# Kernel tuning notes

Hardware: AMD Instinct MI355X
Metric: run time of the kernel (lower is better)

Reference implementation:

```python
import jax, jax.numpy as jnp
import numpy as np

B, D, INNER, OUT = 8192, 256, 64, 256


def setup_inputs() -> dict:
    key = jax.random.key(0)
    ks = jax.random.split(key, 10)
    s = 0.1
    return {
        "x": jax.random.normal(ks[0], (B, D), dtype=jnp.float32),
        # per-feature inner MLPs: Linear(1, inner) -> ReLU -> Linear(inner, 1)
        "w1": jax.random.normal(ks[1], (D, INNER), dtype=jnp.float32) * s,
        "b1": jax.random.normal(ks[2], (D, INNER), dtype=jnp.float32) * s,
        "w2": jax.random.normal(ks[3], (D, INNER), dtype=jnp.float32) * s,
        "b2": jax.random.normal(ks[4], (D,), dtype=jnp.float32) * s,
        # outer MLP: Linear(D, inner) -> ReLU -> Linear(inner, out)
        "wo1": jax.random.normal(ks[5], (INNER, D), dtype=jnp.float32) * s,
        "bo1": jax.random.normal(ks[6], (INNER,), dtype=jnp.float32) * s,
        "wo2": jax.random.normal(ks[7], (OUT, INNER), dtype=jnp.float32) * s,
        "bo2": jax.random.normal(ks[8], (OUT,), dtype=jnp.float32) * s,
    }


def reference(x, w1, b1, w2, b2, wo1, bo1, wo2, bo2):
    # Vectorized per-feature tiny MLPs: h[b,d,i] = relu(x[b,d]*w1[d,i] + b1[d,i])
    h = jax.nn.relu(x[:, :, None] * w1[None, :, :] + b1[None, :, :])  # [B, D, INNER]
    inner = jnp.einsum('bdi,di->bd', h, w2) + b2[None, :]             # [B, D]
    # Outer MLP
    g = jax.nn.relu(inner @ wo1.T + bo1)                              # [B, INNER]
    return g @ wo2.T + bo2                                            # [B, OUT]
```

## Files before the change

kernel.cpp:

```cpp
#include <hip/hip_runtime.h>


#define B_TOT 8192
#define D_DIM 256
#define I_DIM 64
#define O_DIM 256
#define TB 8


__global__ __launch_bounds__(256)
void kal_prep(const float* __restrict__ w1, const float* __restrict__ b1,
              const float* __restrict__ w2, const float* __restrict__ wo1,
              const float* __restrict__ wo2, float4* __restrict__ ws) {
    int idx = blockIdx.x * 256 + threadIdx.x;
    if (idx < 16384) {
        int i = idx >> 8;
        int d = idx & 255;
        ws[idx] = make_float4(w1[d * I_DIM + i], b1[d * I_DIM + i],
                              w2[d * I_DIM + i], 0.0f);
    } else if (idx < 16384 + 4096) {
        int r  = idx - 16384;
        int dd = r >> 6;
        int j  = r & 63;
        ws[idx] = ((const float4*)wo1)[j * (D_DIM / 4) + dd];
    } else if (idx < 16384 + 8192) {
        int r  = idx - (16384 + 4096);
        int jj = r >> 8;
        int o  = r & 255;
        ws[idx] = ((const float4*)wo2)[o * (I_DIM / 4) + jj];
    }
}

__global__ __launch_bounds__(256)
void kal_main(const float* __restrict__ x,  const float* __restrict__ b2,
              const float* __restrict__ bo1, const float* __restrict__ bo2,
              const float4* __restrict__ ws, float* __restrict__ out) {
    const float4* pa = ws;
    const float4* pb = ws + 16384;
    const float4* pc = ws + 16384 + 4096;

    __shared__ float inner_s[TB][D_DIM];
    __shared__ float g_s[TB][I_DIM];

    const int t    = threadIdx.x;
    const int row0 = blockIdx.x * TB;

    {
        const int d = t;
        float xv[TB];
        #pragma unroll
        for (int b = 0; b < TB; ++b)
            xv[b] = x[(row0 + b) * D_DIM + d];

        float acc[TB];
        const float b2v = b2[d];
        #pragma unroll
        for (int b = 0; b < TB; ++b) acc[b] = b2v;

        #pragma unroll 8
        for (int i = 0; i < I_DIM; ++i) {
            const float4 w = pa[i * D_DIM + d];
            #pragma unroll
            for (int b = 0; b < TB; ++b) {
                float h = fmaf(xv[b], w.x, w.y);
                h = fmaxf(h, 0.0f);
                acc[b] = fmaf(h, w.z, acc[b]);
            }
        }
        #pragma unroll
        for (int b = 0; b < TB; ++b) inner_s[b][d] = acc[b];
    }
    __syncthreads();

    {
        const int j   = t & 63;
        const int grp = t >> 6;
        const float bo1v = bo1[j];
        float gacc[TB / 4];
        #pragma unroll
        for (int r = 0; r < TB / 4; ++r) gacc[r] = bo1v;

        #pragma unroll 4
        for (int dd = 0; dd < D_DIM / 4; ++dd) {
            const float4 wv = pb[dd * I_DIM + j];
            #pragma unroll
            for (int r = 0; r < TB / 4; ++r) {
                const int b = grp * (TB / 4) + r;
                float4 iv = ((const float4*)&inner_s[b][0])[dd];
                gacc[r] = fmaf(iv.x, wv.x, gacc[r]);
                gacc[r] = fmaf(iv.y, wv.y, gacc[r]);
                gacc[r] = fmaf(iv.z, wv.z, gacc[r]);
                gacc[r] = fmaf(iv.w, wv.w, gacc[r]);
            }
        }
        #pragma unroll
        for (int r = 0; r < TB / 4; ++r)
            g_s[grp * (TB / 4) + r][j] = fmaxf(gacc[r], 0.0f);
    }
    __syncthreads();

    {
        const int o = t;
        float oacc[TB];
        const float bo2v = bo2[o];
        #pragma unroll
        for (int b = 0; b < TB; ++b) oacc[b] = bo2v;

        #pragma unroll 4
        for (int jj = 0; jj < I_DIM / 4; ++jj) {
            const float4 wv = pc[jj * O_DIM + o];
            #pragma unroll
            for (int b = 0; b < TB; ++b) {
                float4 gv = ((const float4*)&g_s[b][0])[jj];
                oacc[b] = fmaf(gv.x, wv.x, oacc[b]);
                oacc[b] = fmaf(gv.y, wv.y, oacc[b]);
                oacc[b] = fmaf(gv.z, wv.z, oacc[b]);
                oacc[b] = fmaf(gv.w, wv.w, oacc[b]);
            }
        }
        #pragma unroll
        for (int b = 0; b < TB; ++b)
            out[(row0 + b) * O_DIM + o] = oacc[b];
    }
}

extern "C" void kernel_launch(void* const* d_in, const int* in_sizes, int n_in,
                              void* d_out, int out_size, void* d_ws, size_t ws_size,
                              hipStream_t stream) {
    const float* x   = (const float*)d_in[0];
    const float* w1  = (const float*)d_in[1];
    const float* b1  = (const float*)d_in[2];
    const float* w2  = (const float*)d_in[3];
    const float* b2  = (const float*)d_in[4];
    const float* wo1 = (const float*)d_in[5];
    const float* bo1 = (const float*)d_in[6];
    const float* wo2 = (const float*)d_in[7];
    const float* bo2 = (const float*)d_in[8];
    float* out = (float*)d_out;
    float4* ws = (float4*)d_ws;

    kal_prep<<<(24576 + 255) / 256, 256, 0, stream>>>(w1, b1, w2, wo1, wo2, ws);
    kal_main<<<B_TOT / TB, 256, 0, stream>>>(x, b2, bo1, bo2, ws, out);
}
```

Measured before the change: 101.6 us.

## Run outer MLP layers on bf16 MFMA with 16-row blocks

Replaces the scalar FMA loops for the two outer linear layers with bf16 16x16x32 MFMA instructions, pre-converting and re-laying out wo1/wo2 into bf16 fragment order in the prep kernel. Blocks now handle 16 rows with 512 threads, and the inner activations and hidden layer are stored in shared memory as bf16. This removes much of the VALU work outside the per-feature MLP, at the cost of reduced precision in the outer layers.

```diff
diff --git a/kernel.cpp b/kernel.cpp
--- a/kernel.cpp
+++ b/kernel.cpp
@@ -1,11 +1,17 @@
 #include <hip/hip_runtime.h>
+#include <hip/hip_bf16.h>
 
 
 #define B_TOT 8192
 #define D_DIM 256
 #define I_DIM 64
 #define O_DIM 256
-#define TB 8
+#define RB 16
+#define NT 512
+
+typedef __hip_bfloat16 bf16;
+using short8 = __attribute__((ext_vector_type(8))) short;
+using f32x4  = __attribute__((ext_vector_type(4))) float;
 
 
 __global__ __launch_bounds__(256)
@@ -18,109 +24,102 @@
         int d = idx & 255;
         ws[idx] = make_float4(w1[d * I_DIM + i], b1[d * I_DIM + i],
                               w2[d * I_DIM + i], 0.0f);
-    } else if (idx < 16384 + 4096) {
+    } else if (idx < 32768) {
         int r  = idx - 16384;
-        int dd = r >> 6;
-        int j  = r & 63;
-        ws[idx] = ((const float4*)wo1)[j * (D_DIM / 4) + dd];
-    } else if (idx < 16384 + 8192) {
-        int r  = idx - (16384 + 4096);
-        int jj = r >> 8;
-        int o  = r & 255;
-        ws[idx] = ((const float4*)wo2)[o * (I_DIM / 4) + jj];
+        int kc = r >> 11;
+        int rem = r & 2047;
+        int j  = rem >> 5;
+        int kk = rem & 31;
+        bf16* pbB = (bf16*)(ws + 16384);
+        pbB[r] = __float2bfloat16(wo1[j * D_DIM + kc * 32 + kk]);
+    } else if (idx < 49152) {
+        int r  = idx - 32768;
+        int kc = r >> 13;
+        int rem = r & 8191;
+        int o  = rem >> 5;
+        int kk = rem & 31;
+        bf16* pcB = (bf16*)(ws + 16384) + 16384;
+        pcB[r] = __float2bfloat16(wo2[o * I_DIM + kc * 32 + kk]);
     }
 }
 
-__global__ __launch_bounds__(256)
+__global__ __launch_bounds__(NT)
 void kal_main(const float* __restrict__ x,  const float* __restrict__ b2,
               const float* __restrict__ bo1, const float* __restrict__ bo2,
               const float4* __restrict__ ws, float* __restrict__ out) {
-    const float4* pa = ws;
-    const float4* pb = ws + 16384;
-    const float4* pc = ws + 16384 + 4096;
+    const float4* pa  = ws;
+    const bf16*   pbB = (const bf16*)(ws + 16384);
+    const bf16*   pcB = pbB + 16384;
 
-    __shared__ float inner_s[TB][D_DIM];
-    __shared__ float g_s[TB][I_DIM];
+    __shared__ bf16 inner_bf[RB][264];
+    __shared__ bf16 g_bf[RB][72];
 
     const int t    = threadIdx.x;
-    const int row0 = blockIdx.x * TB;
+    const int row0 = blockIdx.x * RB;
 
     {
-        const int d = t;
-        float xv[TB];
-        #pragma unroll
-        for (int b = 0; b < TB; ++b)
-            xv[b] = x[(row0 + b) * D_DIM + d];
-
-        float acc[TB];
+        const int d    = t & 255;
+        const int half = t >> 8;
+        float xv[8], acc[8];
         const float b2v = b2[d];
         #pragma unroll
-        for (int b = 0; b < TB; ++b) acc[b] = b2v;
-
-        #pragma unroll 8
+        for (int b = 0; b < 8; ++b) {
+            xv[b]  = x[(row0 + half * 8 + b) * D_DIM + d];
+            acc[b] = b2v;
+        }
+        #pragma unroll 4
         for (int i = 0; i < I_DIM; ++i) {
             const float4 w = pa[i * D_DIM + d];
             #pragma unroll
-            for (int b = 0; b < TB; ++b) {
+            for (int b = 0; b < 8; ++b) {
                 float h = fmaf(xv[b], w.x, w.y);
                 h = fmaxf(h, 0.0f);
                 acc[b] = fmaf(h, w.z, acc[b]);
             }
         }
         #pragma unroll
-        for (int b = 0; b < TB; ++b) inner_s[b][d] = acc[b];
+        for (int b = 0; b < 8; ++b)
+            inner_bf[half * 8 + b][d] = __float2bfloat16(acc[b]);
     }
     __syncthreads();
 
-    {
-        const int j   = t & 63;
-        const int grp = t >> 6;
-        const float bo1v = bo1[j];
-        float gacc[TB / 4];
+    const int lane = t & 63;
+    const int wave = t >> 6;
+    const int col  = lane & 15;
+    const int quad = lane >> 4;
+
+    if (wave < 4) {
+        const int j0 = wave * 16;
+        f32x4 acc = {0.f, 0.f, 0.f, 0.f};
         #pragma unroll
-        for (int r = 0; r < TB / 4; ++r) gacc[r] = bo1v;
-
-        #pragma unroll 4
-        for (int dd = 0; dd < D_DIM / 4; ++dd) {
-            const float4 wv = pb[dd * I_DIM + j];
-            #pragma unroll
-            for (int r = 0; r < TB / 4; ++r) {
-                const int b = grp * (TB / 4) + r;
-                float4 iv = ((const float4*)&inner_s[b][0])[dd];
-                gacc[r] = fmaf(iv.x, wv.x, gacc[r]);
-                gacc[r] = fmaf(iv.y, wv.y, gacc[r]);
-                gacc[r] = fmaf(iv.z, wv.z, gacc[r]);
-                gacc[r] = fmaf(iv.w, wv.w, gacc[r]);
-            }
+        for (int kc = 0; kc < 8; ++kc) {
+            short8 af = *(const short8*)&inner_bf[col][kc * 32 + quad * 8];
+            short8 bfr = *(const short8*)&pbB[(kc * 64 + j0 + col) * 32 + quad * 8];
+            acc = __builtin_amdgcn_mfma_f32_16x16x32_bf16(af, bfr, acc, 0, 0, 0);
         }
+        const float bo1v = bo1[j0 + col];
         #pragma unroll
-        for (int r = 0; r < TB / 4; ++r)
-            g_s[grp * (TB / 4) + r][j] = fmaxf(gacc[r], 0.0f);
+        for (int r = 0; r < 4; ++r) {
+            const int row = quad * 4 + r;
+            g_bf[row][j0 + col] = __float2bfloat16(fmaxf(acc[r] + bo1v, 0.0f));
+        }
     }
     __syncthreads();
 
-    {
-        const int o = t;
-        float oacc[TB];
-        const float bo2v = bo2[o];
+    #pragma unroll
+    for (int tile = 0; tile < 2; ++tile) {
+        const int o0 = wave * 16 + tile * 128;
+        f32x4 acc = {0.f, 0.f, 0.f, 0.f};
         #pragma unroll
-        for (int b = 0; b < TB; ++b) oacc[b] = bo2v;
-
-        #pragma unroll 4
-        for (int jj = 0; jj < I_DIM / 4; ++jj) {
-            const float4 wv = pc[jj * O_DIM + o];
-            #pragma unroll
-            for (int b = 0; b < TB; ++b) {
-                float4 gv = ((const float4*)&g_s[b][0])[jj];
-                oacc[b] = fmaf(gv.x, wv.x, oacc[b]);
-                oacc[b] = fmaf(gv.y, wv.y, oacc[b]);
-                oacc[b] = fmaf(gv.z, wv.z, oacc[b]);
-                oacc[b] = fmaf(gv.w, wv.w, oacc[b]);
-            }
+        for (int kc = 0; kc < 2; ++kc) {
+            short8 af = *(const short8*)&g_bf[col][kc * 32 + quad * 8];
+            short8 bfr = *(const short8*)&pcB[(kc * 256 + o0 + col) * 32 + quad * 8];
+            acc = __builtin_amdgcn_mfma_f32_16x16x32_bf16(af, bfr, acc, 0, 0, 0);
         }
+        const float bo2v = bo2[o0 + col];
         #pragma unroll
-        for (int b = 0; b < TB; ++b)
-            out[(row0 + b) * O_DIM + o] = oacc[b];
+        for (int r = 0; r < 4; ++r)
+            out[(row0 + quad * 4 + r) * O_DIM + o0 + col] = acc[r] + bo2v;
     }
 }
 
@@ -139,6 +138,6 @@
     float* out = (float*)d_out;
     float4* ws = (float4*)d_ws;
 
-    kal_prep<<<(24576 + 255) / 256, 256, 0, stream>>>(w1, b1, w2, wo1, wo2, ws);
-    kal_main<<<B_TOT / TB, 256, 0, stream>>>(x, b2, bo1, bo2, ws, out);
+    kal_prep<<<(49152 + 255) / 256, 256, 0, stream>>>(w1, b1, w2, wo1, wo2, ws);
+    kal_main<<<B_TOT / RB, NT, 0, stream>>>(x, b2, bo1, bo2, ws, out);
 }
```

Result: faster. 90.29 us (-11.1%).
